# Optimization experiments

Hardware: AMD Instinct MI355X
Metric: run time of the kernel (lower is better)

## Reference

```python
import jax, jax.numpy as jnp
import numpy as np

C = 128
SHAPE = (1, C, 48, 48, 48)  # (N, C, D, H, W)
FILTERS = (1, 3, 3, 3, 1)
INIT_SCALE = 10.0
TAIL_MASS = 1e-9
LIKELIHOOD_BOUND = 1e-9


def setup_inputs() -> dict:
    key = jax.random.key(0)
    ks = jax.random.split(key, 8)
    x = jax.random.normal(ks[0], SHAPE, jnp.float32) * 3.0
    noise = jax.random.uniform(ks[1], SHAPE, jnp.float32)  # shifted to [-0.5,0.5) inside reference
    scale = INIT_SCALE ** (1.0 / (len(FILTERS) - 1))
    inp = {"x": x, "noise": noise}
    for i in range(4):
        init_m = float(np.log(np.expm1(1.0 / scale / FILTERS[i + 1])))
        inp[f"m{i}"] = jnp.full((C, FILTERS[i + 1], FILTERS[i]), init_m, jnp.float32)
        inp[f"b{i}"] = jax.random.uniform(ks[2 + i], (C, FILTERS[i + 1], 1), jnp.float32, -0.5, 0.5)
        if i < 3:
            inp[f"f{i}"] = jnp.zeros((C, FILTERS[i + 1], 1), jnp.float32)
    # quantiles init: [-init_scale, 0, init_scale] per channel, shape (C,1,3)
    inp["quantiles"] = jnp.tile(
        jnp.array([[[-INIT_SCALE, 0.0, INIT_SCALE]]], jnp.float32), (C, 1, 1)
    )
    return inp


def _logits_cumulative(z, mats, biases, factors, stop_gradient=False):
    # z: (C, 1, B); per-channel tiny 4-layer CDF MLP
    sg = jax.lax.stop_gradient if stop_gradient else (lambda t: t)
    for i in range(4):
        m = sg(jax.nn.softplus(mats[i]))          # (C, f_out, f_in)
        z = jnp.matmul(m, z) + sg(biases[i])      # (C, f_out, B)
        if i < 3:
            z = z + sg(jnp.tanh(factors[i])) * jnp.tanh(z)
    return z


def reference(x, noise, m0, m1, m2, m3, b0, b1, b2, b3, f0, f1, f2, quantiles):
    mats = [m0, m1, m2, m3]
    biases = [b0, b1, b2, b3]
    factors = [f0, f1, f2]

    # quantize_mode == 'noise': additive uniform(-0.5, 0.5) noise
    outputs = x + (noise - 0.5)

    n, c, d, h, w = outputs.shape
    z = jnp.transpose(outputs, (1, 0, 2, 3, 4)).reshape(c, 1, -1)  # (C,1,B)
    lower = _logits_cumulative(z - 0.5, mats, biases, factors)
    upper = _logits_cumulative(z + 0.5, mats, biases, factors)
    sign = -jax.lax.stop_gradient(jnp.sign(lower + upper))
    likelihood = jnp.abs(jax.nn.sigmoid(sign * upper) - jax.nn.sigmoid(sign * lower))
    likelihood = jnp.transpose(likelihood.reshape(c, n, d, h, w), (1, 0, 2, 3, 4))
    likelihood = jnp.maximum(likelihood, LIKELIHOOD_BOUND)  # Low_bound forward

    t = float(np.log(2.0 / TAIL_MASS - 1.0))
    target = jnp.array([-t, 0.0, t], jnp.float32)
    logits_q = _logits_cumulative(quantiles, mats, biases, factors, stop_gradient=True)
    quantiles_loss = jnp.sum(jnp.abs(logits_q - target))

    return outputs, likelihood, quantiles_loss
```

## Files before the change

### kernel.cpp

```cpp
#include <hip/hip_runtime.h>
#include <math.h>

#define NCH      128
#define SPATIAL  110592
#define BLOCKS_X 27
#define ELEMS_PER_BLOCK 4096
#define THREADS  256
#define ITERS    4

#define QT 21.416413017506358f

__device__ __forceinline__ float frcp(float x){ return __builtin_amdgcn_rcpf(x); }
__device__ __forceinline__ float ftanh(float x){ return 1.0f - 2.0f*frcp(__expf(2.0f*x) + 1.0f); }
__device__ __forceinline__ float fsig(float x){ return frcp(1.0f + __expf(-x)); }
__device__ __forceinline__ float fsoftplus(float x){ return fmaxf(x, 0.0f) + log1pf(__expf(-fabsf(x))); }

struct Params {
    float w0[3], w1[9], w2[9], w3[3];
    float t0[3], t1[3], t2[3];
    float B0[3], B1[3], B2[3], B3;
};

template<bool USE_F>
__device__ __forceinline__ float eval_mlp(float z, const Params& P){
    float h0 = fmaf(P.w0[0], z, P.B0[0]);
    float h1 = fmaf(P.w0[1], z, P.B0[1]);
    float h2 = fmaf(P.w0[2], z, P.B0[2]);
    if (USE_F){
        h0 = fmaf(P.t0[0], ftanh(h0), h0);
        h1 = fmaf(P.t0[1], ftanh(h1), h1);
        h2 = fmaf(P.t0[2], ftanh(h2), h2);
    }
    float g0 = fmaf(P.w1[0],h0, fmaf(P.w1[1],h1, fmaf(P.w1[2],h2, P.B1[0])));
    float g1 = fmaf(P.w1[3],h0, fmaf(P.w1[4],h1, fmaf(P.w1[5],h2, P.B1[1])));
    float g2 = fmaf(P.w1[6],h0, fmaf(P.w1[7],h1, fmaf(P.w1[8],h2, P.B1[2])));
    if (USE_F){
        g0 = fmaf(P.t1[0], ftanh(g0), g0);
        g1 = fmaf(P.t1[1], ftanh(g1), g1);
        g2 = fmaf(P.t1[2], ftanh(g2), g2);
    }
    h0 = fmaf(P.w2[0],g0, fmaf(P.w2[1],g1, fmaf(P.w2[2],g2, P.B2[0])));
    h1 = fmaf(P.w2[3],g0, fmaf(P.w2[4],g1, fmaf(P.w2[5],g2, P.B2[1])));
    h2 = fmaf(P.w2[6],g0, fmaf(P.w2[7],g1, fmaf(P.w2[8],g2, P.B2[2])));
    if (USE_F){
        h0 = fmaf(P.t2[0], ftanh(h0), h0);
        h1 = fmaf(P.t2[1], ftanh(h1), h1);
        h2 = fmaf(P.t2[2], ftanh(h2), h2);
    }
    return fmaf(P.w3[0],h0, fmaf(P.w3[1],h1, fmaf(P.w3[2],h2, P.B3)));
}

template<bool USE_F>
__device__ __forceinline__ void elem(float xv, float nv, const Params& P, float& o, float& l){
    o = xv + nv - 0.5f;
    float lo = eval_mlp<USE_F>(o - 0.5f, P);
    float hi = eval_mlp<USE_F>(o + 0.5f, P);
    float su = lo + hi;
    float s  = (su < 0.0f) ? 1.0f : ((su > 0.0f) ? -1.0f : 0.0f);
    float a  = fsig(s*hi);
    float b  = fsig(s*lo);
    l = fmaxf(fabsf(a - b), 1e-9f);
}

template<bool USE_F>
__device__ __forceinline__ void run_loop(const float4* __restrict__ x4, const float4* __restrict__ n4,
                                         float4* __restrict__ o4, float4* __restrict__ l4,
                                         int base, int tid, const Params& P){
    #pragma unroll
    for (int it = 0; it < ITERS; ++it){
        int i = base + it*THREADS + tid;
        float4 xv = x4[i];
        float4 nv = n4[i];
        float4 ov, lv;
        elem<USE_F>(xv.x, nv.x, P, ov.x, lv.x);
        elem<USE_F>(xv.y, nv.y, P, ov.y, lv.y);
        elem<USE_F>(xv.z, nv.z, P, ov.z, lv.z);
        elem<USE_F>(xv.w, nv.w, P, ov.w, lv.w);
        o4[i] = ov;
        l4[i] = lv;
    }
}

__global__ __launch_bounds__(THREADS) void eb_main(
    const float* __restrict__ x, const float* __restrict__ noise,
    const float* __restrict__ m0, const float* __restrict__ b0, const float* __restrict__ f0,
    const float* __restrict__ m1, const float* __restrict__ b1, const float* __restrict__ f1,
    const float* __restrict__ m2, const float* __restrict__ b2, const float* __restrict__ f2,
    const float* __restrict__ m3, const float* __restrict__ b3,
    float* __restrict__ out, float* __restrict__ lik)
{
    const int c   = blockIdx.y;
    const int tid = threadIdx.x;

    __shared__ float sp[43];
    if (tid < 43){
        float v;
        if      (tid <  3) v = fsoftplus(m0[c*3 + tid]);
        else if (tid < 12) v = fsoftplus(m1[c*9 + (tid-3)]);
        else if (tid < 21) v = fsoftplus(m2[c*9 + (tid-12)]);
        else if (tid < 24) v = fsoftplus(m3[c*3 + (tid-21)]);
        else if (tid < 27) v = tanhf(f0[c*3 + (tid-24)]);
        else if (tid < 30) v = tanhf(f1[c*3 + (tid-27)]);
        else if (tid < 33) v = tanhf(f2[c*3 + (tid-30)]);
        else if (tid < 36) v = b0[c*3 + (tid-33)];
        else if (tid < 39) v = b1[c*3 + (tid-36)];
        else if (tid < 42) v = b2[c*3 + (tid-39)];
        else               v = b3[c];
        sp[tid] = v;
    }
    __syncthreads();

    Params P;
    #pragma unroll
    for (int j=0;j<3;j++) P.w0[j]=sp[j];
    #pragma unroll
    for (int j=0;j<9;j++) P.w1[j]=sp[3+j];
    #pragma unroll
    for (int j=0;j<9;j++) P.w2[j]=sp[12+j];
    #pragma unroll
    for (int j=0;j<3;j++) P.w3[j]=sp[21+j];
    #pragma unroll
    for (int j=0;j<3;j++) P.t0[j]=sp[24+j];
    #pragma unroll
    for (int j=0;j<3;j++) P.t1[j]=sp[27+j];
    #pragma unroll
    for (int j=0;j<3;j++) P.t2[j]=sp[30+j];
    #pragma unroll
    for (int j=0;j<3;j++) P.B0[j]=sp[33+j];
    #pragma unroll
    for (int j=0;j<3;j++) P.B1[j]=sp[36+j];
    #pragma unroll
    for (int j=0;j<3;j++) P.B2[j]=sp[39+j];
    P.B3 = sp[42];

    bool use_f = false;
    #pragma unroll
    for (int j=0;j<3;j++)
        use_f = use_f || (P.t0[j]!=0.0f) || (P.t1[j]!=0.0f) || (P.t2[j]!=0.0f);

    const float4* x4 = (const float4*)x;
    const float4* n4 = (const float4*)noise;
    float4* o4 = (float4*)out;
    float4* l4 = (float4*)lik;
    const int base = c*(SPATIAL/4) + blockIdx.x*(ELEMS_PER_BLOCK/4);

    if (use_f) run_loop<true >(x4, n4, o4, l4, base, tid, P);
    else       run_loop<false>(x4, n4, o4, l4, base, tid, P);
}

__global__ __launch_bounds__(384) void eb_quant(
    const float* __restrict__ m0, const float* __restrict__ b0, const float* __restrict__ f0,
    const float* __restrict__ m1, const float* __restrict__ b1, const float* __restrict__ f1,
    const float* __restrict__ m2, const float* __restrict__ b2, const float* __restrict__ f2,
    const float* __restrict__ m3, const float* __restrict__ b3,
    const float* __restrict__ q, float* __restrict__ loss)
{
    const int tid = threadIdx.x;
    const int c = tid / 3;
    const int j = tid - c*3;

    Params P;
    #pragma unroll
    for (int k=0;k<3;k++) P.w0[k]=fsoftplus(m0[c*3+k]);
    #pragma unroll
    for (int k=0;k<9;k++) P.w1[k]=fsoftplus(m1[c*9+k]);
    #pragma unroll
    for (int k=0;k<9;k++) P.w2[k]=fsoftplus(m2[c*9+k]);
    #pragma unroll
    for (int k=0;k<3;k++) P.w3[k]=fsoftplus(m3[c*3+k]);
    #pragma unroll
    for (int k=0;k<3;k++) P.t0[k]=tanhf(f0[c*3+k]);
    #pragma unroll
    for (int k=0;k<3;k++) P.t1[k]=tanhf(f1[c*3+k]);
    #pragma unroll
    for (int k=0;k<3;k++) P.t2[k]=tanhf(f2[c*3+k]);
    #pragma unroll
    for (int k=0;k<3;k++) P.B0[k]=b0[c*3+k];
    #pragma unroll
    for (int k=0;k<3;k++) P.B1[k]=b1[c*3+k];
    #pragma unroll
    for (int k=0;k<3;k++) P.B2[k]=b2[c*3+k];
    P.B3 = b3[c];

    float z      = q[c*3 + j];
    float logit  = eval_mlp<true>(z, P);
    float target = (j==0) ? -QT : ((j==1) ? 0.0f : QT);
    float diff   = fabsf(logit - target);

    #pragma unroll
    for (int off = 32; off > 0; off >>= 1)
        diff += __shfl_down(diff, off, 64);

    __shared__ float red[6];
    if ((tid & 63) == 0) red[tid >> 6] = diff;
    __syncthreads();
    if (tid == 0){
        float s = 0.0f;
        #pragma unroll
        for (int i = 0; i < 6; i++) s += red[i];
        *loss = s;
    }
}

extern "C" void kernel_launch(void* const* d_in, const int* in_sizes, int n_in,
                              void* d_out, int out_size, void* d_ws, size_t ws_size,
                              hipStream_t stream) {
    const float* x  = (const float*)d_in[0];
    const float* nz = (const float*)d_in[1];
    const float* m0 = (const float*)d_in[2];
    const float* b0 = (const float*)d_in[3];
    const float* f0 = (const float*)d_in[4];
    const float* m1 = (const float*)d_in[5];
    const float* b1 = (const float*)d_in[6];
    const float* f1 = (const float*)d_in[7];
    const float* m2 = (const float*)d_in[8];
    const float* b2 = (const float*)d_in[9];
    const float* f2 = (const float*)d_in[10];
    const float* m3 = (const float*)d_in[11];
    const float* b3 = (const float*)d_in[12];
    const float* qq = (const float*)d_in[13];

    float* out  = (float*)d_out;
    float* lik  = out + (size_t)NCH*SPATIAL;
    float* loss = lik + (size_t)NCH*SPATIAL;

    dim3 grid(BLOCKS_X, NCH);
    eb_main<<<grid, THREADS, 0, stream>>>(x, nz, m0,b0,f0, m1,b1,f1, m2,b2,f2, m3,b3, out, lik);
    eb_quant<<<1, 384, 0, stream>>>(m0,b0,f0, m1,b1,f1, m2,b2,f2, m3,b3, qq, loss);
}
```

Baseline: 250.3 us.

## Collapse the tanh-free CDF MLP into a per-channel affine map and stream elements

When all tanh factors are zero, the four-layer per-channel MLP is a composition of linear layers. A new prep kernel computes a slope and offset per channel once, plus a flag saying whether any factor is nonzero, and also writes the quantile loss. The main kernel then replaces two full MLP evaluations per element with one fma and one add. It uses a grid-stride loop with next-iteration prefetch and nontemporal stores. A general MLP path is kept for nonzero factors, but it reloads parameters from global memory on every iteration, and eb_main now has to wait for the prep kernel.

New measurement: 231.4 us. -7.6%, faster.

```diff
diff --git a/kernel.cpp b/kernel.cpp
--- a/kernel.cpp
+++ b/kernel.cpp
@@ -3,12 +3,14 @@
 
 #define NCH      128
 #define SPATIAL  110592
-#define BLOCKS_X 27
-#define ELEMS_PER_BLOCK 4096
+#define NV4      3538944
+#define CV4      27648
 #define THREADS  256
-#define ITERS    4
+#define GRID     2048
 
 #define QT 21.416413017506358f
+
+typedef float v4f __attribute__((ext_vector_type(4)));
 
 __device__ __forceinline__ float frcp(float x){ return __builtin_amdgcn_rcpf(x); }
 __device__ __forceinline__ float ftanh(float x){ return 1.0f - 2.0f*frcp(__expf(2.0f*x) + 1.0f); }
@@ -20,6 +22,37 @@
     float t0[3], t1[3], t2[3];
     float B0[3], B1[3], B2[3], B3;
 };
+
+__device__ __forceinline__ Params load_params(int c,
+    const float* __restrict__ m0, const float* __restrict__ b0, const float* __restrict__ f0,
+    const float* __restrict__ m1, const float* __restrict__ b1, const float* __restrict__ f1,
+    const float* __restrict__ m2, const float* __restrict__ b2, const float* __restrict__ f2,
+    const float* __restrict__ m3, const float* __restrict__ b3)
+{
+    Params P;
+    #pragma unroll
+    for (int k=0;k<3;k++) P.w0[k]=fsoftplus(m0[c*3+k]);
+    #pragma unroll
+    for (int k=0;k<9;k++) P.w1[k]=fsoftplus(m1[c*9+k]);
+    #pragma unroll
+    for (int k=0;k<9;k++) P.w2[k]=fsoftplus(m2[c*9+k]);
+    #pragma unroll
+    for (int k=0;k<3;k++) P.w3[k]=fsoftplus(m3[c*3+k]);
+    #pragma unroll
+    for (int k=0;k<3;k++) P.t0[k]=ftanh(f0[c*3+k]);
+    #pragma unroll
+    for (int k=0;k<3;k++) P.t1[k]=ftanh(f1[c*3+k]);
+    #pragma unroll
+    for (int k=0;k<3;k++) P.t2[k]=ftanh(f2[c*3+k]);
+    #pragma unroll
+    for (int k=0;k<3;k++) P.B0[k]=b0[c*3+k];
+    #pragma unroll
+    for (int k=0;k<3;k++) P.B1[k]=b1[c*3+k];
+    #pragma unroll
+    for (int k=0;k<3;k++) P.B2[k]=b2[c*3+k];
+    P.B3 = b3[c];
+    return P;
+}
 
 template<bool USE_F>
 __device__ __forceinline__ float eval_mlp(float z, const Params& P){
@@ -50,137 +83,37 @@
     return fmaf(P.w3[0],h0, fmaf(P.w3[1],h1, fmaf(P.w3[2],h2, P.B3)));
 }
 
-template<bool USE_F>
-__device__ __forceinline__ void elem(float xv, float nv, const Params& P, float& o, float& l){
-    o = xv + nv - 0.5f;
-    float lo = eval_mlp<USE_F>(o - 0.5f, P);
-    float hi = eval_mlp<USE_F>(o + 0.5f, P);
+__device__ __forceinline__ float lik_from_logits(float lo, float hi){
     float su = lo + hi;
-    float s  = (su < 0.0f) ? 1.0f : ((su > 0.0f) ? -1.0f : 0.0f);
+    float s  = (su > 0.0f) ? -1.0f : ((su < 0.0f) ? 1.0f : 0.0f);
     float a  = fsig(s*hi);
     float b  = fsig(s*lo);
-    l = fmaxf(fabsf(a - b), 1e-9f);
-}
-
-template<bool USE_F>
-__device__ __forceinline__ void run_loop(const float4* __restrict__ x4, const float4* __restrict__ n4,
-                                         float4* __restrict__ o4, float4* __restrict__ l4,
-                                         int base, int tid, const Params& P){
-    #pragma unroll
-    for (int it = 0; it < ITERS; ++it){
-        int i = base + it*THREADS + tid;
-        float4 xv = x4[i];
-        float4 nv = n4[i];
-        float4 ov, lv;
-        elem<USE_F>(xv.x, nv.x, P, ov.x, lv.x);
-        elem<USE_F>(xv.y, nv.y, P, ov.y, lv.y);
-        elem<USE_F>(xv.z, nv.z, P, ov.z, lv.z);
-        elem<USE_F>(xv.w, nv.w, P, ov.w, lv.w);
-        o4[i] = ov;
-        l4[i] = lv;
-    }
-}
-
-__global__ __launch_bounds__(THREADS) void eb_main(
-    const float* __restrict__ x, const float* __restrict__ noise,
+    return fmaxf(fabsf(a - b), 1e-9f);
+}
+
+__global__ __launch_bounds__(384) void eb_prep(
     const float* __restrict__ m0, const float* __restrict__ b0, const float* __restrict__ f0,
     const float* __restrict__ m1, const float* __restrict__ b1, const float* __restrict__ f1,
     const float* __restrict__ m2, const float* __restrict__ b2, const float* __restrict__ f2,
     const float* __restrict__ m3, const float* __restrict__ b3,
-    float* __restrict__ out, float* __restrict__ lik)
-{
-    const int c   = blockIdx.y;
-    const int tid = threadIdx.x;
-
-    __shared__ float sp[43];
-    if (tid < 43){
-        float v;
-        if      (tid <  3) v = fsoftplus(m0[c*3 + tid]);
-        else if (tid < 12) v = fsoftplus(m1[c*9 + (tid-3)]);
-        else if (tid < 21) v = fsoftplus(m2[c*9 + (tid-12)]);
-        else if (tid < 24) v = fsoftplus(m3[c*3 + (tid-21)]);
-        else if (tid < 27) v = tanhf(f0[c*3 + (tid-24)]);
-        else if (tid < 30) v = tanhf(f1[c*3 + (tid-27)]);
-        else if (tid < 33) v = tanhf(f2[c*3 + (tid-30)]);
-        else if (tid < 36) v = b0[c*3 + (tid-33)];
-        else if (tid < 39) v = b1[c*3 + (tid-36)];
-        else if (tid < 42) v = b2[c*3 + (tid-39)];
-        else               v = b3[c];
-        sp[tid] = v;
-    }
-    __syncthreads();
-
-    Params P;
-    #pragma unroll
-    for (int j=0;j<3;j++) P.w0[j]=sp[j];
-    #pragma unroll
-    for (int j=0;j<9;j++) P.w1[j]=sp[3+j];
-    #pragma unroll
-    for (int j=0;j<9;j++) P.w2[j]=sp[12+j];
-    #pragma unroll
-    for (int j=0;j<3;j++) P.w3[j]=sp[21+j];
-    #pragma unroll
-    for (int j=0;j<3;j++) P.t0[j]=sp[24+j];
-    #pragma unroll
-    for (int j=0;j<3;j++) P.t1[j]=sp[27+j];
-    #pragma unroll
-    for (int j=0;j<3;j++) P.t2[j]=sp[30+j];
-    #pragma unroll
-    for (int j=0;j<3;j++) P.B0[j]=sp[33+j];
-    #pragma unroll
-    for (int j=0;j<3;j++) P.B1[j]=sp[36+j];
-    #pragma unroll
-    for (int j=0;j<3;j++) P.B2[j]=sp[39+j];
-    P.B3 = sp[42];
-
-    bool use_f = false;
-    #pragma unroll
-    for (int j=0;j<3;j++)
-        use_f = use_f || (P.t0[j]!=0.0f) || (P.t1[j]!=0.0f) || (P.t2[j]!=0.0f);
-
-    const float4* x4 = (const float4*)x;
-    const float4* n4 = (const float4*)noise;
-    float4* o4 = (float4*)out;
-    float4* l4 = (float4*)lik;
-    const int base = c*(SPATIAL/4) + blockIdx.x*(ELEMS_PER_BLOCK/4);
-
-    if (use_f) run_loop<true >(x4, n4, o4, l4, base, tid, P);
-    else       run_loop<false>(x4, n4, o4, l4, base, tid, P);
-}
-
-__global__ __launch_bounds__(384) void eb_quant(
-    const float* __restrict__ m0, const float* __restrict__ b0, const float* __restrict__ f0,
-    const float* __restrict__ m1, const float* __restrict__ b1, const float* __restrict__ f1,
-    const float* __restrict__ m2, const float* __restrict__ b2, const float* __restrict__ f2,
-    const float* __restrict__ m3, const float* __restrict__ b3,
-    const float* __restrict__ q, float* __restrict__ loss)
+    const float* __restrict__ q, float* __restrict__ loss,
+    float2* __restrict__ ab, int* __restrict__ flag)
 {
     const int tid = threadIdx.x;
     const int c = tid / 3;
     const int j = tid - c*3;
 
-    Params P;
-    #pragma unroll
-    for (int k=0;k<3;k++) P.w0[k]=fsoftplus(m0[c*3+k]);
-    #pragma unroll
-    for (int k=0;k<9;k++) P.w1[k]=fsoftplus(m1[c*9+k]);
-    #pragma unroll
-    for (int k=0;k<9;k++) P.w2[k]=fsoftplus(m2[c*9+k]);
-    #pragma unroll
-    for (int k=0;k<3;k++) P.w3[k]=fsoftplus(m3[c*3+k]);
-    #pragma unroll
-    for (int k=0;k<3;k++) P.t0[k]=tanhf(f0[c*3+k]);
-    #pragma unroll
-    for (int k=0;k<3;k++) P.t1[k]=tanhf(f1[c*3+k]);
-    #pragma unroll
-    for (int k=0;k<3;k++) P.t2[k]=tanhf(f2[c*3+k]);
-    #pragma unroll
-    for (int k=0;k<3;k++) P.B0[k]=b0[c*3+k];
-    #pragma unroll
-    for (int k=0;k<3;k++) P.B1[k]=b1[c*3+k];
-    #pragma unroll
-    for (int k=0;k<3;k++) P.B2[k]=b2[c*3+k];
-    P.B3 = b3[c];
+    Params P = load_params(c, m0,b0,f0, m1,b1,f1, m2,b2,f2, m3,b3);
+
+    bool anyf = false;
+    #pragma unroll
+    for (int k=0;k<3;k++)
+        anyf = anyf || (P.t0[k]!=0.0f) || (P.t1[k]!=0.0f) || (P.t2[k]!=0.0f);
+
+    __shared__ int sf;
+    if (tid == 0) sf = 0;
+    __syncthreads();
+    if (anyf) sf = 1;
 
     float z      = q[c*3 + j];
     float logit  = eval_mlp<true>(z, P);
@@ -199,6 +132,85 @@
         #pragma unroll
         for (int i = 0; i < 6; i++) s += red[i];
         *loss = s;
+        *flag = sf;
+    }
+
+    if (j == 0){
+        float B = eval_mlp<false>(0.0f, P);
+        float A = eval_mlp<false>(1.0f, P) - B;
+        ab[c] = make_float2(A, B - 0.5f*A);
+    }
+}
+
+__global__ __launch_bounds__(THREADS) void eb_main(
+    const float* __restrict__ x, const float* __restrict__ noise,
+    const float* __restrict__ m0, const float* __restrict__ b0, const float* __restrict__ f0,
+    const float* __restrict__ m1, const float* __restrict__ b1, const float* __restrict__ f1,
+    const float* __restrict__ m2, const float* __restrict__ b2, const float* __restrict__ f2,
+    const float* __restrict__ m3, const float* __restrict__ b3,
+    const float2* __restrict__ ab, const int* __restrict__ flag,
+    float* __restrict__ out, float* __restrict__ lik)
+{
+    __shared__ float sA[NCH], sBl[NCH];
+    __shared__ int sflag;
+    const int tid = threadIdx.x;
+    if (tid < NCH){ float2 v = ab[tid]; sA[tid] = v.x; sBl[tid] = v.y; }
+    if (tid == 0) sflag = *flag;
+    __syncthreads();
+    const bool use_f = (sflag != 0);
+
+    const v4f* __restrict__ x4 = (const v4f*)x;
+    const v4f* __restrict__ n4 = (const v4f*)noise;
+    v4f* __restrict__ o4 = (v4f*)out;
+    v4f* __restrict__ l4 = (v4f*)lik;
+
+    int i = blockIdx.x*THREADS + tid;
+    const int stride = GRID*THREADS;
+
+    if (!use_f){
+        v4f xa = x4[i], na = n4[i];
+        while (true){
+            const int inext = i + stride;
+            const bool vnext = inext < NV4;
+            v4f xb, nb;
+            if (vnext){ xb = x4[inext]; nb = n4[inext]; }
+
+            const int c = i / CV4;
+            const float A  = sA[c];
+            const float Bl = sBl[c];
+
+            v4f ov, lv;
+            #pragma unroll
+            for (int e = 0; e < 4; ++e){
+                float o  = xa[e] + na[e] - 0.5f;
+                float lo = fmaf(A, o, Bl);
+                float hi = lo + A;
+                ov[e] = o;
+                lv[e] = lik_from_logits(lo, hi);
+            }
+            __builtin_nontemporal_store(ov, o4 + i);
+            __builtin_nontemporal_store(lv, l4 + i);
+
+            if (!vnext) break;
+            i = inext; xa = xb; na = nb;
+        }
+    } else {
+        for (; i < NV4; i += stride){
+            const int c = i / CV4;
+            Params P = load_params(c, m0,b0,f0, m1,b1,f1, m2,b2,f2, m3,b3);
+            v4f xv = x4[i], nv = n4[i];
+            v4f ov, lv;
+            #pragma unroll
+            for (int e = 0; e < 4; ++e){
+                float o  = xv[e] + nv[e] - 0.5f;
+                float lo = eval_mlp<true>(o - 0.5f, P);
+                float hi = eval_mlp<true>(o + 0.5f, P);
+                ov[e] = o;
+                lv[e] = lik_from_logits(lo, hi);
+            }
+            __builtin_nontemporal_store(ov, o4 + i);
+            __builtin_nontemporal_store(lv, l4 + i);
+        }
     }
 }
 
@@ -224,7 +236,10 @@
     float* lik  = out + (size_t)NCH*SPATIAL;
     float* loss = lik + (size_t)NCH*SPATIAL;
 
-    dim3 grid(BLOCKS_X, NCH);
-    eb_main<<<grid, THREADS, 0, stream>>>(x, nz, m0,b0,f0, m1,b1,f1, m2,b2,f2, m3,b3, out, lik);
-    eb_quant<<<1, 384, 0, stream>>>(m0,b0,f0, m1,b1,f1, m2,b2,f2, m3,b3, qq, loss);
-}
+    float2* ab  = (float2*)d_ws;
+    int*   flag = (int*)((char*)d_ws + NCH*sizeof(float2));
+
+    eb_prep<<<1, 384, 0, stream>>>(m0,b0,f0, m1,b1,f1, m2,b2,f2, m3,b3, qq, loss, ab, flag);
+    eb_main<<<GRID, THREADS, 0, stream>>>(x, nz, m0,b0,f0, m1,b1,f1, m2,b2,f2, m3,b3,
+                                          ab, flag, out, lik);
+}
```
